# Performance work log

Hardware: AMD Instinct MI355X
Metric: run time of the kernel (lower is better)

The kernel has to match this reference:

```python
import jax, jax.numpy as jnp
import numpy as np

B, N_CAPS, N_VOTES, D_IN, D_H, D_CP = 1024, 64, 36, 256, 128, 32
TWO_PI = 2.0 * np.pi


def geometric_transform(pose):
    # pose: [..., 6] -> affine 3x3 matrix [..., 3, 3] (nonlinear, full affine)
    sx, sy, theta, shear, tx, ty = jnp.split(pose, 6, axis=-1)
    sx = jax.nn.sigmoid(sx) + 1e-2
    sy = jax.nn.sigmoid(sy) + 1e-2
    tx = jnp.tanh(tx * 5.0)
    ty = jnp.tanh(ty * 5.0)
    shear = jnp.tanh(shear * 5.0)
    theta = theta * TWO_PI
    c, s = jnp.cos(theta), jnp.sin(theta)
    row0 = jnp.concatenate([sx * c + shear * sy * s, -sx * s + shear * sy * c, tx], -1)
    row1 = jnp.concatenate([sy * s, sy * c, ty], -1)
    zeros = jnp.zeros_like(tx)
    row2 = jnp.concatenate([zeros, zeros, jnp.ones_like(tx)], -1)
    return jnp.stack([row0, row1, row2], axis=-2)


def setup_inputs() -> dict:
    key = jax.random.key(0)
    ks = jax.random.split(key, 16)
    u = lambda k, shp: 0.5 * (jax.random.uniform(k, shp, jnp.float32) - 0.5)
    return {
        "features": jax.random.normal(ks[0], (B, N_CAPS, D_IN), jnp.float32),
        "w1": u(ks[1], (1, N_CAPS, D_IN, D_H)),
        "b1": jnp.zeros((1, N_CAPS, 1, D_H), jnp.float32),
        "w2": u(ks[2], (1, N_CAPS, D_H, D_CP)),
        "b2": jnp.zeros((1, N_CAPS, 1, D_CP), jnp.float32),
        "caps_mlp_w": u(ks[3], (1, N_CAPS, D_CP + 1, D_H)),
        "caps_mlp_b": jnp.zeros((1, N_CAPS, 1, D_H), jnp.float32),
        "cpr_dynamic_w": u(ks[4], (1, N_CAPS, D_H, N_VOTES * 6)),
        "ccr_w": u(ks[5], (1, N_CAPS, D_H, 6)),
        "ccr_b": jnp.zeros((1, N_CAPS, 1, 6), jnp.float32),
        "pres_caps_w": u(ks[6], (1, N_CAPS, D_H, 1)),
        "pres_caps_b": jnp.zeros((1, N_CAPS, 1, 1), jnp.float32),
        "pres_vote_w": u(ks[7], (1, N_CAPS, D_H, N_VOTES)),
        "pres_vote_b": jnp.zeros((1, N_CAPS, 1, N_VOTES), jnp.float32),
        "scale_vote_w": u(ks[8], (1, N_CAPS, D_H, N_VOTES)),
        "scale_vote_b": jnp.zeros((1, N_CAPS, 1, N_VOTES), jnp.float32),
        "cpr_static": jax.random.uniform(ks[9], (1, N_CAPS, N_VOTES, 6), jnp.float32) - 0.5,
    }


def reference(features, w1, b1, w2, b2, caps_mlp_w, caps_mlp_b, cpr_dynamic_w,
              ccr_w, ccr_b, pres_caps_w, pres_caps_b, pres_vote_w, pres_vote_b,
              scale_vote_w, scale_vote_b, cpr_static):
    batch_size = features.shape[0]
    x = features[:, :, None, :]                               # [B, C, 1, 256]
    h = jax.nn.relu(x @ w1 + b1)                              # [B, C, 1, H]
    raw_caps_params = jax.nn.relu(h @ w2 + b2)                # [B, C, 1, P]
    caps_exist = jnp.ones(raw_caps_params.shape[:-1] + (1,), raw_caps_params.dtype)
    caps_params = jnp.concatenate([raw_caps_params, caps_exist], -1)  # [B, C, 1, P+1]
    caps_feat = jax.nn.relu(caps_params @ caps_mlp_w + caps_mlp_b)    # [B, C, 1, H]

    cpr_dynamic = (caps_feat @ cpr_dynamic_w).reshape(batch_size, N_CAPS, N_VOTES, 6)
    ccr = caps_feat @ ccr_w + ccr_b                           # [B, C, 1, 6]
    pres_logit_per_caps = (caps_feat @ pres_caps_w + pres_caps_b)[:, :, 0, :]   # [B, C, 1]
    pres_logit_per_vote = (caps_feat @ pres_vote_w + pres_vote_b)[:, :, 0, :]   # [B, C, V]
    scale_per_vote = (caps_feat @ scale_vote_w + scale_vote_b)[:, :, 0, :]      # [B, C, V]

    ccr_mat = geometric_transform(ccr)                        # [B, C, 1, 3, 3]
    cpr_mat = geometric_transform(cpr_dynamic + cpr_static)   # [B, C, V, 3, 3]
    votes = ccr_mat @ cpr_mat                                 # [B, C, V, 3, 3]

    pres_per_caps = jax.nn.sigmoid(pres_logit_per_caps)
    pres_per_vote = pres_per_caps * jax.nn.sigmoid(pres_logit_per_vote)
    scale_per_vote = jax.nn.softplus(scale_per_vote + 0.5) + 0.01
    dynamic_weights_l2 = jnp.sum(cpr_dynamic ** 2) / batch_size / 2.0
    return (votes, scale_per_vote, pres_per_vote, pres_logit_per_caps,
            pres_logit_per_vote, dynamic_weights_l2, raw_caps_params[:, :, 0, :], features)
```

## Files before the change

kernel.cpp:

```cpp
#include <hip/hip_runtime.h>
#include <math.h>

#define NB   1024
#define NC   64
#define DIN  256
#define DH   128
#define DCP  32
#define NV   36

#define OFF0 0
#define OFF1 21233664
#define OFF2 23592960
#define OFF3 25952256
#define OFF4 26017792
#define OFF5 28377088
#define OFF6 28377089
#define OFF7 30474241

#define SM_FST 0
#define SM_R2  4608
#define SM_R3  8960
#define SM_TOT 10112

#define SM_XS  SM_R2
#define SM_W1C (SM_R2 + 576)
#define SM_W2S SM_R2
#define SM_WM  SM_R2
#define SM_WH  SM_R2
#define SM_HD  (SM_R2 + 1280)
#define SM_HB  (SM_R2 + 3872)
#define SM_WD  SM_R2
#define SM_DYN SM_R2
#define SM_CPS SM_R3
#define SM_M   SM_R3
#define SM_PSIG (SM_R3 + 192)

__device__ __forceinline__ float sigm(float x) { return 1.0f / (1.0f + __expf(-x)); }
__device__ __forceinline__ float tanh5(float x) {
    x = fminf(fmaxf(5.0f * x, -15.0f), 15.0f);
    float z = __expf(2.0f * x);
    return (z - 1.0f) / (z + 1.0f);
}
__device__ __forceinline__ void geo(const float* p, float* m) {
    float sx = sigm(p[0]) + 0.01f;
    float sy = sigm(p[1]) + 0.01f;
    float th = p[2] * 6.28318530717958647692f;
    float sh = tanh5(p[3]);
    float tx = tanh5(p[4]);
    float ty = tanh5(p[5]);
    float cc = __cosf(th), ss = __sinf(th);
    m[0] =  sx * cc + sh * sy * ss;
    m[1] = -sx * ss + sh * sy * cc;
    m[2] = tx;
    m[3] = sy * ss;
    m[4] = sy * cc;
    m[5] = ty;
}

__global__ void zero_l2_kernel(float* out) { out[OFF5] = 0.0f; }

__global__ __launch_bounds__(256, 4)
void caps_fused_kernel(const float* __restrict__ feat,
                       const float* __restrict__ w1,  const float* __restrict__ b1,
                       const float* __restrict__ w2,  const float* __restrict__ b2,
                       const float* __restrict__ wm,  const float* __restrict__ bm,
                       const float* __restrict__ wdy,
                       const float* __restrict__ wccr,const float* __restrict__ bccr,
                       const float* __restrict__ wpc, const float* __restrict__ bpc,
                       const float* __restrict__ wpv, const float* __restrict__ bpv,
                       const float* __restrict__ wsv, const float* __restrict__ bsv,
                       const float* __restrict__ cst,
                       float* __restrict__ out)
{
    __shared__ float sm[SM_TOT];
    const int t  = threadIdx.x;
    const int c  = blockIdx.y;
    const int rb = blockIdx.x * 32;
    const int t4 = t * 4;

    float4 w2pf[4];

    {
        const int tx = t & 31;
        const int ty = t >> 5;
        const int xrow = t >> 3, xk2 = (t & 7) * 2;
        const float* fsrc = &feat[(rb + xrow) * (NC * DIN) + c * DIN + xk2];
        const float* w1b_ = &w1[c * (DIN * DH)];
        float2 xr  = *(const float2*)fsrc;
        float4 wra = *(const float4*)(w1b_ + t4);
        float4 wrb = *(const float4*)(w1b_ + 1024 + t4);
        float acc[4][4] = {};
        for (int k0 = 0; k0 < DIN; k0 += 16) {
            __syncthreads();
            sm[SM_XS + xk2 * 36 + xrow]       = xr.x;
            sm[SM_XS + (xk2 + 1) * 36 + xrow] = xr.y;
            *(float4*)&sm[SM_W1C + t4]        = wra;
            *(float4*)&sm[SM_W1C + 1024 + t4] = wrb;
            __syncthreads();
            if (k0 + 16 < DIN) {
                xr  = *(const float2*)(fsrc + k0 + 16);
                wra = *(const float4*)(w1b_ + (k0 + 16) * DH + t4);
                wrb = *(const float4*)(w1b_ + (k0 + 16) * DH + 1024 + t4);
            } else {
#pragma unroll
                for (int p = 0; p < 4; ++p)
                    w2pf[p] = *(const float4*)&w2[c * (DH * DCP) + (t + p * 256) * 4];
            }
#pragma unroll
            for (int kk = 0; kk < 16; ++kk) {
                const float4 av = *(const float4*)&sm[SM_XS + kk * 36 + ty * 4];
                const float4 bv = *(const float4*)&sm[SM_W1C + kk * DH + tx * 4];
                acc[0][0] += av.x * bv.x; acc[0][1] += av.x * bv.y; acc[0][2] += av.x * bv.z; acc[0][3] += av.x * bv.w;
                acc[1][0] += av.y * bv.x; acc[1][1] += av.y * bv.y; acc[1][2] += av.y * bv.z; acc[1][3] += av.y * bv.w;
                acc[2][0] += av.z * bv.x; acc[2][1] += av.z * bv.y; acc[2][2] += av.z * bv.z; acc[2][3] += av.z * bv.w;
                acc[3][0] += av.w * bv.x; acc[3][1] += av.w * bv.y; acc[3][2] += av.w * bv.z; acc[3][3] += av.w * bv.w;
            }
        }
        const float4 bb = *(const float4*)&b1[c * DH + tx * 4];
        const float bbA[4] = { bb.x, bb.y, bb.z, bb.w };
#pragma unroll
        for (int j = 0; j < 4; ++j) {
            float4 vv;
            vv.x = fmaxf(acc[0][j] + bbA[j], 0.0f);
            vv.y = fmaxf(acc[1][j] + bbA[j], 0.0f);
            vv.z = fmaxf(acc[2][j] + bbA[j], 0.0f);
            vv.w = fmaxf(acc[3][j] + bbA[j], 0.0f);
            *(float4*)&sm[SM_FST + (tx * 4 + j) * 36 + ty * 4] = vv;
        }
    }

    __syncthreads();
#pragma unroll
    for (int p = 0; p < 4; ++p)
        *(float4*)&sm[SM_W2S + t4 + p * 1024] = w2pf[p];
    __syncthreads();
    float4 wmpf[5];
    {
#pragma unroll
        for (int p = 0; p < 5; ++p) {
            const int idx = t + p * 256;
            if (idx < 1056)
                wmpf[p] = *(const float4*)&wm[c * (33 * DH) + idx * 4];
        }
        const int b  = t & 31;
        const int j4 = (t >> 5) << 2;
        float acc[4] = {};
#pragma unroll 8
        for (int k = 0; k < DH; ++k) {
            const float h = sm[SM_FST + k * 36 + b];
            const float4 wv = *(const float4*)&sm[SM_W2S + k * DCP + j4];
            acc[0] += h * wv.x; acc[1] += h * wv.y; acc[2] += h * wv.z; acc[3] += h * wv.w;
        }
        const float4 b2v = *(const float4*)&b2[c * DCP + j4];
        const float b2A[4] = { b2v.x, b2v.y, b2v.z, b2v.w };
#pragma unroll
        for (int jj = 0; jj < 4; ++jj) {
            const float v = fmaxf(acc[jj] + b2A[jj], 0.0f);
            out[OFF6 + ((rb + b) * NC + c) * DCP + j4 + jj] = v;
            sm[SM_CPS + b * 36 + j4 + jj] = v;
        }
    }

    __syncthreads();
#pragma unroll
    for (int p = 0; p < 5; ++p) {
        const int idx = t + p * 256;
        if (idx < 1056)
            *(float4*)&sm[SM_WM + idx * 4] = wmpf[p];
    }
    __syncthreads();
    const float* d2p[5]; int d2adv[5]; float d2msk[5], d2pf[5];
#pragma unroll
    for (int p = 0; p < 5; ++p) {
        const int idx = t + p * 256;
        const int kp = idx / 80, colp = idx - kp * 80;
        const float* s; int st; float mk = 1.0f;
        if (colp < 6)       { s = &wccr[c * (DH * 6) + kp * 6 + colp];          st = 6;  }
        else if (colp == 6) { s = &wpc [c * DH + kp];                            st = 1;  }
        else if (colp < 43) { s = &wpv [c * (DH * NV) + kp * NV + (colp - 7)];   st = NV; }
        else if (colp < 79) { s = &wsv [c * (DH * NV) + kp * NV + (colp - 43)];  st = NV; }
        else                { s = &wccr[c * (DH * 6)]; st = 0; mk = 0.0f; }
        d2pf[p]  = *s;
        d2p[p]   = s + st * 16;
        d2adv[p] = st * 16;
        d2msk[p] = mk;
    }
    float bpf = 0.0f;
    if (t < 80) {
        if (t < 6)       bpf = bccr[c * 6 + t];
        else if (t == 6) bpf = bpc[c];
        else if (t < 43) bpf = bpv[c * NV + (t - 7)];
        else if (t < 79) bpf = bsv[c * NV + (t - 43)];
    }
    {
        const int b  = t & 31;
        const int nb = (t >> 5) << 4;
        float acc[16] = {};
#pragma unroll
        for (int k4 = 0; k4 < 8; ++k4) {
            const float4 a4 = *(const float4*)&sm[SM_CPS + b * 36 + k4 * 4];
            const float aA[4] = { a4.x, a4.y, a4.z, a4.w };
#pragma unroll
            for (int kk = 0; kk < 4; ++kk) {
                const int k = k4 * 4 + kk;
#pragma unroll
                for (int jq = 0; jq < 4; ++jq) {
                    const float4 wv = *(const float4*)&sm[SM_WM + k * DH + nb + jq * 4];
                    acc[jq*4+0] += aA[kk] * wv.x; acc[jq*4+1] += aA[kk] * wv.y;
                    acc[jq*4+2] += aA[kk] * wv.z; acc[jq*4+3] += aA[kk] * wv.w;
                }
            }
        }
#pragma unroll
        for (int jq = 0; jq < 4; ++jq) {
            const float4 wv = *(const float4*)&sm[SM_WM + 32 * DH + nb + jq * 4];
            acc[jq*4+0] += wv.x; acc[jq*4+1] += wv.y; acc[jq*4+2] += wv.z; acc[jq*4+3] += wv.w;
        }
#pragma unroll
        for (int jq = 0; jq < 4; ++jq) {
            const float4 bmv = *(const float4*)&bm[c * DH + nb + jq * 4];
            sm[SM_FST + (nb + jq*4 + 0) * 36 + b] = fmaxf(acc[jq*4+0] + bmv.x, 0.0f);
            sm[SM_FST + (nb + jq*4 + 1) * 36 + b] = fmaxf(acc[jq*4+1] + bmv.y, 0.0f);
            sm[SM_FST + (nb + jq*4 + 2) * 36 + b] = fmaxf(acc[jq*4+2] + bmv.z, 0.0f);
            sm[SM_FST + (nb + jq*4 + 3) * 36 + b] = fmaxf(acc[jq*4+3] + bmv.w, 0.0f);
        }
    }

    {
        const int txx = t & 15;
        const int tyy = t >> 4;
        float acc[2][5] = {};
        for (int k0 = 0; k0 < DH; k0 += 16) {
            __syncthreads();
#pragma unroll
            for (int p = 0; p < 5; ++p)
                sm[SM_WH + t + p * 256] = d2msk[p] * d2pf[p];
            if (k0 == 0 && t < 80) sm[SM_HB + t] = bpf;
            __syncthreads();
            if (k0 + 16 < DH) {
#pragma unroll
                for (int p = 0; p < 5; ++p) {
                    d2pf[p] = *d2p[p];
                    d2p[p] += d2adv[p];
                }
            }
#pragma unroll
            for (int kk = 0; kk < 16; ++kk) {
                const float2 av = *(const float2*)&sm[SM_FST + (k0 + kk) * 36 + tyy * 2];
#pragma unroll
                for (int j = 0; j < 5; ++j) {
                    const float w = sm[SM_WH + kk * 80 + txx * 5 + j];
                    acc[0][j] += av.x * w;
                    acc[1][j] += av.y * w;
                }
            }
        }
#pragma unroll
        for (int i = 0; i < 2; ++i)
#pragma unroll
            for (int j = 0; j < 5; ++j)
                sm[SM_HD + (tyy * 2 + i) * 81 + txx * 5 + j] = acc[i][j];
    }

    const float* d4p[7]; int d4dst[7]; unsigned d4v = 0; float2 d4pf[7];
    {
        const float* wdyb = &wdy[c * (DH * 216)];
#pragma unroll
        for (int p = 0; p < 7; ++p) {
            const int e2  = (t + p * 256) * 2;
            const int row = e2 / 224, col = e2 - row * 224;
            d4dst[p] = row * 224 + col;
            d4pf[p]  = make_float2(0.0f, 0.0f);
            d4p[p]   = wdyb;
            if (col < 216) {
                d4v |= 1u << p;
                d4p[p]  = wdyb + row * 216 + col;
                d4pf[p] = *(const float2*)d4p[p];
                d4p[p] += 16 * 216;
            }
        }
    }
    __syncthreads();

    if (t < 32) {
        const int b = t;
        const float plc = sm[SM_HD + b * 81 + 6] + sm[SM_HB + 6];
        out[OFF3 + (rb + b) * NC + c] = plc;
        sm[SM_PSIG + b] = sigm(plc);
        float pp[6], m[6];
#pragma unroll
        for (int i = 0; i < 6; ++i) pp[i] = sm[SM_HD + b * 81 + i] + sm[SM_HB + i];
        geo(pp, m);
#pragma unroll
        for (int i = 0; i < 6; ++i) sm[SM_M + b * 6 + i] = m[i];
    }
    __syncthreads();

#pragma unroll
    for (int p = 0; p < 10; ++p) {
        const int item = t + p * 256;
        const int b = item / 80, col = item % 80;
        if (col >= 7 && col < 79) {
            const float v = sm[SM_HD + b * 81 + col] + sm[SM_HB + col];
            const int base = ((rb + b) * NC + c) * NV;
            if (col < 43) {
                const int o = col - 7;
                out[OFF4 + base + o] = v;
                out[OFF2 + base + o] = sm[SM_PSIG + b] * sigm(v);
            } else {
                const int o = col - 43;
                float sp = v + 0.5f;
                sp = (sp > 15.0f) ? sp : log1pf(__expf(sp));
                out[OFF1 + base + o] = sp + 0.01f;
            }
        }
    }

    float l2loc = 0.0f;
    {
        const int g   = t & 63;
        const int ty4 = t >> 6;
        float acc[8][4] = {};
        for (int k0 = 0; k0 < DH; k0 += 16) {
            __syncthreads();
#pragma unroll
            for (int p = 0; p < 7; ++p)
                *(float2*)&sm[SM_WD + d4dst[p]] = d4pf[p];
            __syncthreads();
            if (k0 + 16 < DH) {
#pragma unroll
                for (int p = 0; p < 7; ++p) {
                    if ((d4v >> p) & 1) {
                        d4pf[p] = *(const float2*)d4p[p];
                        d4p[p] += 16 * 216;
                    }
                }
            }
#pragma unroll
            for (int kk = 0; kk < 16; ++kk) {
                const float4 a0 = *(const float4*)&sm[SM_FST + (k0 + kk) * 36 + ty4 * 8];
                const float4 a1 = *(const float4*)&sm[SM_FST + (k0 + kk) * 36 + ty4 * 8 + 4];
                const float4 w  = *(const float4*)&sm[SM_WD + kk * 224 + g * 4];
                acc[0][0] += a0.x * w.x; acc[0][1] += a0.x * w.y; acc[0][2] += a0.x * w.z; acc[0][3] += a0.x * w.w;
                acc[1][0] += a0.y * w.x; acc[1][1] += a0.y * w.y; acc[1][2] += a0.y * w.z; acc[1][3] += a0.y * w.w;
                acc[2][0] += a0.z * w.x; acc[2][1] += a0.z * w.y; acc[2][2] += a0.z * w.z; acc[2][3] += a0.z * w.w;
                acc[3][0] += a0.w * w.x; acc[3][1] += a0.w * w.y; acc[3][2] += a0.w * w.z; acc[3][3] += a0.w * w.w;
                acc[4][0] += a1.x * w.x; acc[4][1] += a1.x * w.y; acc[4][2] += a1.x * w.z; acc[4][3] += a1.x * w.w;
                acc[5][0] += a1.y * w.x; acc[5][1] += a1.y * w.y; acc[5][2] += a1.y * w.z; acc[5][3] += a1.y * w.w;
                acc[6][0] += a1.z * w.x; acc[6][1] += a1.z * w.y; acc[6][2] += a1.z * w.z; acc[6][3] += a1.z * w.w;
                acc[7][0] += a1.w * w.x; acc[7][1] += a1.w * w.y; acc[7][2] += a1.w * w.z; acc[7][3] += a1.w * w.w;
            }
        }
        for (int half = 0; half < 2; ++half) {
            __syncthreads();
            if (g < 54 && (g >= 27) == (half == 1)) {
#pragma unroll
                for (int i = 0; i < 8; ++i)
#pragma unroll
                    for (int j = 0; j < 4; ++j)
                        sm[SM_DYN + (ty4 * 8 + i) * 109 + (g * 4 + j - half * 108)] = acc[i][j];
            }
            __syncthreads();
#pragma unroll
            for (int p = 0; p < 3; ++p) {
                const int item = t + p * 256;
                if (item < 576) {
                    const int b = item / 18, vh = item % 18;
                    const int v = half * 18 + vh;
                    float dyn[6], pose[6], mB[6];
                    float ss = 0.0f;
#pragma unroll
                    for (int j = 0; j < 6; ++j) {
                        dyn[j] = sm[SM_DYN + b * 109 + vh * 6 + j];
                        ss += dyn[j] * dyn[j];
                        pose[j] = dyn[j] + cst[c * (NV * 6) + v * 6 + j];
                    }
                    l2loc += ss;
                    geo(pose, mB);
                    const float A0 = sm[SM_M + b * 6 + 0], A1 = sm[SM_M + b * 6 + 1];
                    const float A2 = sm[SM_M + b * 6 + 2], A3 = sm[SM_M + b * 6 + 3];
                    const float A4 = sm[SM_M + b * 6 + 4], A5 = sm[SM_M + b * 6 + 5];
                    const int ob = (((rb + b) * NC + c) * NV + v) * 9;
                    out[OFF0 + ob + 0] = A0 * mB[0] + A1 * mB[3];
                    out[OFF0 + ob + 1] = A0 * mB[1] + A1 * mB[4];
                    out[OFF0 + ob + 2] = A0 * mB[2] + A1 * mB[5] + A2;
                    out[OFF0 + ob + 3] = A3 * mB[0] + A4 * mB[3];
                    out[OFF0 + ob + 4] = A3 * mB[1] + A4 * mB[4];
                    out[OFF0 + ob + 5] = A3 * mB[2] + A4 * mB[5] + A5;
                    out[OFF0 + ob + 6] = 0.0f;
                    out[OFF0 + ob + 7] = 0.0f;
                    out[OFF0 + ob + 8] = 1.0f;
                }
            }
        }
    }

    l2loc += __shfl_down(l2loc, 32, 64);
    l2loc += __shfl_down(l2loc, 16, 64);
    l2loc += __shfl_down(l2loc, 8, 64);
    l2loc += __shfl_down(l2loc, 4, 64);
    l2loc += __shfl_down(l2loc, 2, 64);
    l2loc += __shfl_down(l2loc, 1, 64);
    if ((t & 63) == 0) atomicAdd(&out[OFF5], l2loc * (1.0f / 2048.0f));
}

extern "C" void kernel_launch(void* const* d_in, const int* in_sizes, int n_in,
                              void* d_out, int out_size, void* d_ws, size_t ws_size,
                              hipStream_t stream)
{
    const float* feat = (const float*)d_in[0];
    const float* w1   = (const float*)d_in[1];
    const float* b1   = (const float*)d_in[2];
    const float* w2   = (const float*)d_in[3];
    const float* b2   = (const float*)d_in[4];
    const float* wm   = (const float*)d_in[5];
    const float* bm   = (const float*)d_in[6];
    const float* wdy  = (const float*)d_in[7];
    const float* wccr = (const float*)d_in[8];
    const float* bccr = (const float*)d_in[9];
    const float* wpc  = (const float*)d_in[10];
    const float* bpc  = (const float*)d_in[11];
    const float* wpv  = (const float*)d_in[12];
    const float* bpv  = (const float*)d_in[13];
    const float* wsv  = (const float*)d_in[14];
    const float* bsv  = (const float*)d_in[15];
    const float* cst  = (const float*)d_in[16];
    float* out = (float*)d_out;

    zero_l2_kernel<<<1, 1, 0, stream>>>(out);
    hipMemcpyAsync((void*)(out + OFF7), (const void*)feat,
                   (size_t)NB * NC * DIN * sizeof(float),
                   hipMemcpyDeviceToDevice, stream);
    dim3 grid(NB / 32, NC);
    caps_fused_kernel<<<grid, 256, 0, stream>>>(feat, w1, b1, w2, b2, wm, bm, wdy,
                                                wccr, bccr, wpc, bpc, wpv, bpv,
                                                wsv, bsv, cst, out);
}
```

Baseline: 653.8 us.

## Split first GEMM over K halves, transpose head weights, fuse feature copy kernel

The first layer GEMM now splits the K dimension across two 128-thread halves. Each thread computes an 8x4 tile, and the two halves' partial sums are combined through an XOR-swizzled shared-memory reduction. The head-weight staging is transposed so the inner loop reads float4 weights and does four K steps per load. The caps_params output is now written with a coalesced pass from shared memory, and the memset plus device-to-device memcpy are replaced by one grid-stride copy kernel. The aim is fewer LDS reads per FMA, better coalescing and less launch overhead, at the cost of extra syncs and a reduction step.

```diff
diff --git a/kernel.cpp b/kernel.cpp
--- a/kernel.cpp
+++ b/kernel.cpp
@@ -24,11 +24,12 @@
 
 #define SM_XS  SM_R2
 #define SM_W1C (SM_R2 + 576)
+#define SM_RED SM_R2
 #define SM_W2S SM_R2
 #define SM_WM  SM_R2
-#define SM_WH  SM_R2
-#define SM_HD  (SM_R2 + 1280)
-#define SM_HB  (SM_R2 + 3872)
+#define SM_WHT SM_R2
+#define SM_HD  (SM_R2 + 1600)
+#define SM_HB  (SM_R2 + 4192)
 #define SM_WD  SM_R2
 #define SM_DYN SM_R2
 #define SM_CPS SM_R3
@@ -57,7 +58,15 @@
     m[5] = ty;
 }
 
-__global__ void zero_l2_kernel(float* out) { out[OFF5] = 0.0f; }
+__global__ __launch_bounds__(256)
+void prep_kernel(const float* __restrict__ feat, float* __restrict__ out)
+{
+    if (blockIdx.x == 0 && threadIdx.x == 0) out[OFF5] = 0.0f;
+    const int n = NB * NC * DIN;
+    const int stride = gridDim.x * 256;
+    for (int i = blockIdx.x * 256 + threadIdx.x; i < n; i += stride)
+        out[OFF7 + i] = feat[i];
+}
 
 __global__ __launch_bounds__(256, 4)
 void caps_fused_kernel(const float* __restrict__ feat,
@@ -76,63 +85,94 @@
     const int t  = threadIdx.x;
     const int c  = blockIdx.y;
     const int rb = blockIdx.x * 32;
-    const int t4 = t * 4;
 
     float4 w2pf[4];
 
     {
-        const int tx = t & 31;
-        const int ty = t >> 5;
-        const int xrow = t >> 3, xk2 = (t & 7) * 2;
-        const float* fsrc = &feat[(rb + xrow) * (NC * DIN) + c * DIN + xk2];
-        const float* w1b_ = &w1[c * (DIN * DH)];
-        float2 xr  = *(const float2*)fsrc;
-        float4 wra = *(const float4*)(w1b_ + t4);
-        float4 wrb = *(const float4*)(w1b_ + 1024 + t4);
-        float acc[4][4] = {};
-        for (int k0 = 0; k0 < DIN; k0 += 16) {
-            __syncthreads();
-            sm[SM_XS + xk2 * 36 + xrow]       = xr.x;
-            sm[SM_XS + (xk2 + 1) * 36 + xrow] = xr.y;
-            *(float4*)&sm[SM_W1C + t4]        = wra;
-            *(float4*)&sm[SM_W1C + 1024 + t4] = wrb;
-            __syncthreads();
-            if (k0 + 16 < DIN) {
-                xr  = *(const float2*)(fsrc + k0 + 16);
-                wra = *(const float4*)(w1b_ + (k0 + 16) * DH + t4);
-                wrb = *(const float4*)(w1b_ + (k0 + 16) * DH + 1024 + t4);
+        const int kh  = t >> 7;
+        const int tid = t & 127;
+        const int rg  = tid >> 5;
+        const int cg  = tid & 31;
+        const int xrow = tid >> 2;
+        const int xk2  = (tid & 3) * 2;
+        const int wrow = tid >> 4;
+        const int wcol = (tid & 15) * 8;
+        const float* fsrc = &feat[(rb + xrow) * (NC * DIN) + c * DIN + kh * 128 + xk2];
+        const float* wsrc = &w1[c * (DIN * DH) + (kh * 128 + wrow) * DH + wcol];
+        float2 xr = *(const float2*)fsrc;
+        float4 wa = *(const float4*)wsrc;
+        float4 wb = *(const float4*)(wsrc + 4);
+        float acc[8][4] = {};
+        const int xbase = SM_XS  + kh * 288;
+        const int wbase = SM_W1C + kh * 1056;
+        for (int k0 = 0; k0 < 128; k0 += 8) {
+            __syncthreads();
+            sm[xbase + xk2 * 36 + xrow]       = xr.x;
+            sm[xbase + (xk2 + 1) * 36 + xrow] = xr.y;
+            *(float4*)&sm[wbase + wrow * 132 + wcol]     = wa;
+            *(float4*)&sm[wbase + wrow * 132 + wcol + 4] = wb;
+            __syncthreads();
+            if (k0 + 8 < 128) {
+                xr = *(const float2*)(fsrc + k0 + 8);
+                wa = *(const float4*)(wsrc + (k0 + 8) * DH);
+                wb = *(const float4*)(wsrc + (k0 + 8) * DH + 4);
             } else {
 #pragma unroll
                 for (int p = 0; p < 4; ++p)
                     w2pf[p] = *(const float4*)&w2[c * (DH * DCP) + (t + p * 256) * 4];
             }
 #pragma unroll
-            for (int kk = 0; kk < 16; ++kk) {
-                const float4 av = *(const float4*)&sm[SM_XS + kk * 36 + ty * 4];
-                const float4 bv = *(const float4*)&sm[SM_W1C + kk * DH + tx * 4];
-                acc[0][0] += av.x * bv.x; acc[0][1] += av.x * bv.y; acc[0][2] += av.x * bv.z; acc[0][3] += av.x * bv.w;
-                acc[1][0] += av.y * bv.x; acc[1][1] += av.y * bv.y; acc[1][2] += av.y * bv.z; acc[1][3] += av.y * bv.w;
-                acc[2][0] += av.z * bv.x; acc[2][1] += av.z * bv.y; acc[2][2] += av.z * bv.z; acc[2][3] += av.z * bv.w;
-                acc[3][0] += av.w * bv.x; acc[3][1] += av.w * bv.y; acc[3][2] += av.w * bv.z; acc[3][3] += av.w * bv.w;
-            }
-        }
-        const float4 bb = *(const float4*)&b1[c * DH + tx * 4];
-        const float bbA[4] = { bb.x, bb.y, bb.z, bb.w };
-#pragma unroll
-        for (int j = 0; j < 4; ++j) {
-            float4 vv;
-            vv.x = fmaxf(acc[0][j] + bbA[j], 0.0f);
-            vv.y = fmaxf(acc[1][j] + bbA[j], 0.0f);
-            vv.z = fmaxf(acc[2][j] + bbA[j], 0.0f);
-            vv.w = fmaxf(acc[3][j] + bbA[j], 0.0f);
-            *(float4*)&sm[SM_FST + (tx * 4 + j) * 36 + ty * 4] = vv;
-        }
-    }
-
-    __syncthreads();
-#pragma unroll
-    for (int p = 0; p < 4; ++p)
-        *(float4*)&sm[SM_W2S + t4 + p * 1024] = w2pf[p];
+            for (int kk = 0; kk < 8; ++kk) {
+                const float4 a0 = *(const float4*)&sm[xbase + kk * 36 + rg * 8];
+                const float4 a1 = *(const float4*)&sm[xbase + kk * 36 + rg * 8 + 4];
+                const float4 bv = *(const float4*)&sm[wbase + kk * 132 + cg * 4];
+                acc[0][0] += a0.x * bv.x; acc[0][1] += a0.x * bv.y; acc[0][2] += a0.x * bv.z; acc[0][3] += a0.x * bv.w;
+                acc[1][0] += a0.y * bv.x; acc[1][1] += a0.y * bv.y; acc[1][2] += a0.y * bv.z; acc[1][3] += a0.y * bv.w;
+                acc[2][0] += a0.z * bv.x; acc[2][1] += a0.z * bv.y; acc[2][2] += a0.z * bv.z; acc[2][3] += a0.z * bv.w;
+                acc[3][0] += a0.w * bv.x; acc[3][1] += a0.w * bv.y; acc[3][2] += a0.w * bv.z; acc[3][3] += a0.w * bv.w;
+                acc[4][0] += a1.x * bv.x; acc[4][1] += a1.x * bv.y; acc[4][2] += a1.x * bv.z; acc[4][3] += a1.x * bv.w;
+                acc[5][0] += a1.y * bv.x; acc[5][1] += a1.y * bv.y; acc[5][2] += a1.y * bv.z; acc[5][3] += a1.y * bv.w;
+                acc[6][0] += a1.z * bv.x; acc[6][1] += a1.z * bv.y; acc[6][2] += a1.z * bv.z; acc[6][3] += a1.z * bv.w;
+                acc[7][0] += a1.w * bv.x; acc[7][1] += a1.w * bv.y; acc[7][2] += a1.w * bv.z; acc[7][3] += a1.w * bv.w;
+            }
+        }
+        __syncthreads();
+        if (kh == 1) {
+#pragma unroll
+            for (int r = 0; r < 8; ++r) {
+                float4 v = make_float4(acc[r][0], acc[r][1], acc[r][2], acc[r][3]);
+                *(float4*)&sm[SM_RED + tid * 32 + ((r ^ (tid & 7)) << 2)] = v;
+            }
+        }
+        __syncthreads();
+        if (kh == 0) {
+            const float4 bb = *(const float4*)&b1[c * DH + cg * 4];
+            const float bbA[4] = { bb.x, bb.y, bb.z, bb.w };
+#pragma unroll
+            for (int r = 0; r < 8; ++r) {
+                const float4 v = *(const float4*)&sm[SM_RED + tid * 32 + ((r ^ (tid & 7)) << 2)];
+                acc[r][0] = fmaxf(acc[r][0] + v.x + bbA[0], 0.0f);
+                acc[r][1] = fmaxf(acc[r][1] + v.y + bbA[1], 0.0f);
+                acc[r][2] = fmaxf(acc[r][2] + v.z + bbA[2], 0.0f);
+                acc[r][3] = fmaxf(acc[r][3] + v.w + bbA[3], 0.0f);
+            }
+#pragma unroll
+            for (int j = 0; j < 4; ++j) {
+                float4 lo = make_float4(acc[0][j], acc[1][j], acc[2][j], acc[3][j]);
+                float4 hi = make_float4(acc[4][j], acc[5][j], acc[6][j], acc[7][j]);
+                *(float4*)&sm[SM_FST + (cg * 4 + j) * 36 + rg * 8]     = lo;
+                *(float4*)&sm[SM_FST + (cg * 4 + j) * 36 + rg * 8 + 4] = hi;
+            }
+        }
+    }
+
+    __syncthreads();
+    {
+        const int t4 = t * 4;
+#pragma unroll
+        for (int p = 0; p < 4; ++p)
+            *(float4*)&sm[SM_W2S + t4 + p * 1024] = w2pf[p];
+    }
     __syncthreads();
     float4 wmpf[5];
     {
@@ -154,11 +194,8 @@
         const float4 b2v = *(const float4*)&b2[c * DCP + j4];
         const float b2A[4] = { b2v.x, b2v.y, b2v.z, b2v.w };
 #pragma unroll
-        for (int jj = 0; jj < 4; ++jj) {
-            const float v = fmaxf(acc[jj] + b2A[jj], 0.0f);
-            out[OFF6 + ((rb + b) * NC + c) * DCP + j4 + jj] = v;
-            sm[SM_CPS + b * 36 + j4 + jj] = v;
-        }
+        for (int jj = 0; jj < 4; ++jj)
+            sm[SM_CPS + b * 36 + j4 + jj] = fmaxf(acc[jj] + b2A[jj], 0.0f);
     }
 
     __syncthreads();
@@ -168,12 +205,19 @@
         if (idx < 1056)
             *(float4*)&sm[SM_WM + idx * 4] = wmpf[p];
     }
-    __syncthreads();
-    const float* d2p[5]; int d2adv[5]; float d2msk[5], d2pf[5];
+#pragma unroll
+    for (int p = 0; p < 4; ++p) {
+        const int item = t + p * 256;
+        const int b = item >> 5, j = item & 31;
+        out[OFF6 + ((rb + b) * NC + c) * DCP + j] = sm[SM_CPS + b * 36 + j];
+    }
+    __syncthreads();
+    const float* d2p[5]; int d2adv[5], d2dst[5]; float d2msk[5], d2pf[5];
 #pragma unroll
     for (int p = 0; p < 5; ++p) {
         const int idx = t + p * 256;
         const int kp = idx / 80, colp = idx - kp * 80;
+        d2dst[p] = colp * 20 + kp;
         const float* s; int st; float mk = 1.0f;
         if (colp < 6)       { s = &wccr[c * (DH * 6) + kp * 6 + colp];          st = 6;  }
         else if (colp == 6) { s = &wpc [c * DH + kp];                            st = 1;  }
@@ -234,7 +278,7 @@
             __syncthreads();
 #pragma unroll
             for (int p = 0; p < 5; ++p)
-                sm[SM_WH + t + p * 256] = d2msk[p] * d2pf[p];
+                sm[SM_WHT + d2dst[p]] = d2msk[p] * d2pf[p];
             if (k0 == 0 && t < 80) sm[SM_HB + t] = bpf;
             __syncthreads();
             if (k0 + 16 < DH) {
@@ -245,13 +289,16 @@
                 }
             }
 #pragma unroll
-            for (int kk = 0; kk < 16; ++kk) {
-                const float2 av = *(const float2*)&sm[SM_FST + (k0 + kk) * 36 + tyy * 2];
+            for (int kb = 0; kb < 16; kb += 4) {
+                float2 av[4];
+#pragma unroll
+                for (int q = 0; q < 4; ++q)
+                    av[q] = *(const float2*)&sm[SM_FST + (k0 + kb + q) * 36 + tyy * 2];
 #pragma unroll
                 for (int j = 0; j < 5; ++j) {
-                    const float w = sm[SM_WH + kk * 80 + txx * 5 + j];
-                    acc[0][j] += av.x * w;
-                    acc[1][j] += av.y * w;
+                    const float4 wv = *(const float4*)&sm[SM_WHT + (txx * 5 + j) * 20 + kb];
+                    acc[0][j] += av[0].x * wv.x + av[1].x * wv.y + av[2].x * wv.z + av[3].x * wv.w;
+                    acc[1][j] += av[0].y * wv.x + av[1].y * wv.y + av[2].y * wv.z + av[3].y * wv.w;
                 }
             }
         }
@@ -427,10 +474,7 @@
     const float* cst  = (const float*)d_in[16];
     float* out = (float*)d_out;
 
-    zero_l2_kernel<<<1, 1, 0, stream>>>(out);
-    hipMemcpyAsync((void*)(out + OFF7), (const void*)feat,
-                   (size_t)NB * NC * DIN * sizeof(float),
-                   hipMemcpyDeviceToDevice, stream);
+    prep_kernel<<<2048, 256, 0, stream>>>(feat, out);
     dim3 grid(NB / 32, NC);
     caps_fused_kernel<<<grid, 256, 0, stream>>>(feat, w1, b1, w2, b2, wm, bm, wdy,
                                                 wccr, bccr, wpc, bpc, wpv, bpv,
```

Measured after the change: 755.6 us. 1.16x slower.

## Double rows per block to 64 and replace memcpy with a copy kernel

Applied to the files above, without the earlier changes.

Each block now handles 64 batch rows with 512 threads instead of 32 rows with 256 threads. Every per-capsule weight tile loaded into shared memory is therefore reused across twice as many rows, which roughly halves global weight traffic and per-block staging overhead. The zero kernel and device-to-device memcpy are merged into one grid-stride copy kernel. The caps_params output is now written through shared memory in a coalesced pattern. The trade-off is a larger shared-memory footprint, which may lower the number of resident blocks per CU, plus more masking logic in the load loops.

```diff
diff --git a/kernel.cpp b/kernel.cpp
--- a/kernel.cpp
+++ b/kernel.cpp
@@ -17,23 +17,27 @@
 #define OFF6 28377089
 #define OFF7 30474241
 
+#define RT   64
+#define THR  512
+
+#define FSS  68
 #define SM_FST 0
-#define SM_R2  4608
-#define SM_R3  8960
-#define SM_TOT 10112
+#define SM_R2  8704
+#define SM_R3  15680
+#define SM_TOT 17984
 
 #define SM_XS  SM_R2
-#define SM_W1C (SM_R2 + 576)
+#define SM_W1C (SM_R2 + 1088)
 #define SM_W2S SM_R2
 #define SM_WM  SM_R2
 #define SM_WH  SM_R2
 #define SM_HD  (SM_R2 + 1280)
-#define SM_HB  (SM_R2 + 3872)
+#define SM_HB  (SM_R2 + 6464)
 #define SM_WD  SM_R2
 #define SM_DYN SM_R2
 #define SM_CPS SM_R3
 #define SM_M   SM_R3
-#define SM_PSIG (SM_R3 + 192)
+#define SM_PSIG (SM_R3 + 384)
 
 __device__ __forceinline__ float sigm(float x) { return 1.0f / (1.0f + __expf(-x)); }
 __device__ __forceinline__ float tanh5(float x) {
@@ -57,9 +61,17 @@
     m[5] = ty;
 }
 
-__global__ void zero_l2_kernel(float* out) { out[OFF5] = 0.0f; }
-
-__global__ __launch_bounds__(256, 4)
+__global__ __launch_bounds__(256)
+void prep_kernel(const float* __restrict__ feat, float* __restrict__ out)
+{
+    if (blockIdx.x == 0 && threadIdx.x == 0) out[OFF5] = 0.0f;
+    const int n = NB * NC * DIN;
+    const int stride = gridDim.x * 256;
+    for (int i = blockIdx.x * 256 + threadIdx.x; i < n; i += stride)
+        out[OFF7 + i] = feat[i];
+}
+
+__global__ __launch_bounds__(THR, 4)
 void caps_fused_kernel(const float* __restrict__ feat,
                        const float* __restrict__ w1,  const float* __restrict__ b1,
                        const float* __restrict__ w2,  const float* __restrict__ b2,
@@ -75,41 +87,37 @@
     __shared__ float sm[SM_TOT];
     const int t  = threadIdx.x;
     const int c  = blockIdx.y;
-    const int rb = blockIdx.x * 32;
-    const int t4 = t * 4;
-
-    float4 w2pf[4];
+    const int rb = blockIdx.x * RT;
+
+    float4 w2pf[2];
 
     {
         const int tx = t & 31;
         const int ty = t >> 5;
-        const int xrow = t >> 3, xk2 = (t & 7) * 2;
+        const int xrow = t >> 3;
+        const int xk2  = (t & 7) * 2;
         const float* fsrc = &feat[(rb + xrow) * (NC * DIN) + c * DIN + xk2];
-        const float* w1b_ = &w1[c * (DIN * DH)];
-        float2 xr  = *(const float2*)fsrc;
-        float4 wra = *(const float4*)(w1b_ + t4);
-        float4 wrb = *(const float4*)(w1b_ + 1024 + t4);
+        const float* wsrc = &w1[c * (DIN * DH) + (t >> 5) * DH + (t & 31) * 4];
+        float2 xr = *(const float2*)fsrc;
+        float4 wr = *(const float4*)wsrc;
         float acc[4][4] = {};
         for (int k0 = 0; k0 < DIN; k0 += 16) {
             __syncthreads();
-            sm[SM_XS + xk2 * 36 + xrow]       = xr.x;
-            sm[SM_XS + (xk2 + 1) * 36 + xrow] = xr.y;
-            *(float4*)&sm[SM_W1C + t4]        = wra;
-            *(float4*)&sm[SM_W1C + 1024 + t4] = wrb;
+            sm[SM_XS + xk2 * FSS + xrow]       = xr.x;
+            sm[SM_XS + (xk2 + 1) * FSS + xrow] = xr.y;
+            *(float4*)&sm[SM_W1C + (t >> 5) * 128 + (t & 31) * 4] = wr;
             __syncthreads();
             if (k0 + 16 < DIN) {
-                xr  = *(const float2*)(fsrc + k0 + 16);
-                wra = *(const float4*)(w1b_ + (k0 + 16) * DH + t4);
-                wrb = *(const float4*)(w1b_ + (k0 + 16) * DH + 1024 + t4);
+                xr = *(const float2*)(fsrc + k0 + 16);
+                wr = *(const float4*)(wsrc + (k0 + 16) * DH);
             } else {
-#pragma unroll
-                for (int p = 0; p < 4; ++p)
-                    w2pf[p] = *(const float4*)&w2[c * (DH * DCP) + (t + p * 256) * 4];
+                w2pf[0] = *(const float4*)&w2[c * (DH * DCP) + t * 4];
+                w2pf[1] = *(const float4*)&w2[c * (DH * DCP) + (t + THR) * 4];
             }
 #pragma unroll
             for (int kk = 0; kk < 16; ++kk) {
-                const float4 av = *(const float4*)&sm[SM_XS + kk * 36 + ty * 4];
-                const float4 bv = *(const float4*)&sm[SM_W1C + kk * DH + tx * 4];
+                const float4 av = *(const float4*)&sm[SM_XS + kk * FSS + ty * 4];
+                const float4 bv = *(const float4*)&sm[SM_W1C + kk * 128 + tx * 4];
                 acc[0][0] += av.x * bv.x; acc[0][1] += av.x * bv.y; acc[0][2] += av.x * bv.z; acc[0][3] += av.x * bv.w;
                 acc[1][0] += av.y * bv.x; acc[1][1] += av.y * bv.y; acc[1][2] += av.y * bv.z; acc[1][3] += av.y * bv.w;
                 acc[2][0] += av.z * bv.x; acc[2][1] += av.z * bv.y; acc[2][2] += av.z * bv.z; acc[2][3] += av.z * bv.w;
@@ -125,65 +133,72 @@
             vv.y = fmaxf(acc[1][j] + bbA[j], 0.0f);
             vv.z = fmaxf(acc[2][j] + bbA[j], 0.0f);
             vv.w = fmaxf(acc[3][j] + bbA[j], 0.0f);
-            *(float4*)&sm[SM_FST + (tx * 4 + j) * 36 + ty * 4] = vv;
-        }
-    }
-
-    __syncthreads();
-#pragma unroll
-    for (int p = 0; p < 4; ++p)
-        *(float4*)&sm[SM_W2S + t4 + p * 1024] = w2pf[p];
-    __syncthreads();
-    float4 wmpf[5];
-    {
-#pragma unroll
-        for (int p = 0; p < 5; ++p) {
-            const int idx = t + p * 256;
+            *(float4*)&sm[SM_FST + (tx * 4 + j) * FSS + ty * 4] = vv;
+        }
+    }
+
+    __syncthreads();
+    *(float4*)&sm[SM_W2S + t * 4]         = w2pf[0];
+    *(float4*)&sm[SM_W2S + (t + THR) * 4] = w2pf[1];
+    __syncthreads();
+    float4 wmpf[3];
+    {
+#pragma unroll
+        for (int p = 0; p < 3; ++p) {
+            const int idx = t + p * THR;
             if (idx < 1056)
                 wmpf[p] = *(const float4*)&wm[c * (33 * DH) + idx * 4];
         }
-        const int b  = t & 31;
-        const int j4 = (t >> 5) << 2;
+        const int b  = t & 63;
+        const int j4 = (t >> 6) << 2;
         float acc[4] = {};
 #pragma unroll 8
         for (int k = 0; k < DH; ++k) {
-            const float h = sm[SM_FST + k * 36 + b];
+            const float h = sm[SM_FST + k * FSS + b];
             const float4 wv = *(const float4*)&sm[SM_W2S + k * DCP + j4];
             acc[0] += h * wv.x; acc[1] += h * wv.y; acc[2] += h * wv.z; acc[3] += h * wv.w;
         }
         const float4 b2v = *(const float4*)&b2[c * DCP + j4];
-        const float b2A[4] = { b2v.x, b2v.y, b2v.z, b2v.w };
-#pragma unroll
-        for (int jj = 0; jj < 4; ++jj) {
-            const float v = fmaxf(acc[jj] + b2A[jj], 0.0f);
-            out[OFF6 + ((rb + b) * NC + c) * DCP + j4 + jj] = v;
-            sm[SM_CPS + b * 36 + j4 + jj] = v;
-        }
-    }
-
-    __syncthreads();
-#pragma unroll
-    for (int p = 0; p < 5; ++p) {
-        const int idx = t + p * 256;
+        float4 cv;
+        cv.x = fmaxf(acc[0] + b2v.x, 0.0f);
+        cv.y = fmaxf(acc[1] + b2v.y, 0.0f);
+        cv.z = fmaxf(acc[2] + b2v.z, 0.0f);
+        cv.w = fmaxf(acc[3] + b2v.w, 0.0f);
+        *(float4*)&sm[SM_CPS + b * 36 + j4] = cv;
+    }
+
+    __syncthreads();
+#pragma unroll
+    for (int p = 0; p < 3; ++p) {
+        const int idx = t + p * THR;
         if (idx < 1056)
             *(float4*)&sm[SM_WM + idx * 4] = wmpf[p];
     }
-    __syncthreads();
-    const float* d2p[5]; int d2adv[5]; float d2msk[5], d2pf[5];
-#pragma unroll
-    for (int p = 0; p < 5; ++p) {
-        const int idx = t + p * 256;
-        const int kp = idx / 80, colp = idx - kp * 80;
-        const float* s; int st; float mk = 1.0f;
-        if (colp < 6)       { s = &wccr[c * (DH * 6) + kp * 6 + colp];          st = 6;  }
-        else if (colp == 6) { s = &wpc [c * DH + kp];                            st = 1;  }
-        else if (colp < 43) { s = &wpv [c * (DH * NV) + kp * NV + (colp - 7)];   st = NV; }
-        else if (colp < 79) { s = &wsv [c * (DH * NV) + kp * NV + (colp - 43)];  st = NV; }
-        else                { s = &wccr[c * (DH * 6)]; st = 0; mk = 0.0f; }
-        d2pf[p]  = *s;
-        d2p[p]   = s + st * 16;
-        d2adv[p] = st * 16;
-        d2msk[p] = mk;
+#pragma unroll
+    for (int p = 0; p < 4; ++p) {
+        const int item = t + p * THR;
+        const int b = item >> 5, j = item & 31;
+        out[OFF6 + ((rb + b) * NC + c) * DCP + j] = sm[SM_CPS + b * 36 + j];
+    }
+    __syncthreads();
+    const float* d2p[3]; int d2adv[3]; float d2msk[3], d2pf[3];
+#pragma unroll
+    for (int p = 0; p < 3; ++p) {
+        const int idx = t + p * THR;
+        d2pf[p] = 0.0f; d2p[p] = wccr; d2adv[p] = 0; d2msk[p] = 0.0f;
+        if (idx < 1280) {
+            const int kp = idx / 80, colp = idx - kp * 80;
+            const float* s; int st; float mk = 1.0f;
+            if (colp < 6)       { s = &wccr[c * (DH * 6) + kp * 6 + colp];          st = 6;  }
+            else if (colp == 6) { s = &wpc [c * DH + kp];                            st = 1;  }
+            else if (colp < 43) { s = &wpv [c * (DH * NV) + kp * NV + (colp - 7)];   st = NV; }
+            else if (colp < 79) { s = &wsv [c * (DH * NV) + kp * NV + (colp - 43)];  st = NV; }
+            else                { s = &wccr[c * (DH * 6)]; st = 0; mk = 0.0f; }
+            d2pf[p]  = *s;
+            d2p[p]   = s + st * 16;
+            d2adv[p] = st * 16;
+            d2msk[p] = mk;
+        }
     }
     float bpf = 0.0f;
     if (t < 80) {
@@ -193,8 +208,8 @@
         else if (t < 79) bpf = bsv[c * NV + (t - 43)];
     }
     {
-        const int b  = t & 31;
-        const int nb = (t >> 5) << 4;
+        const int b  = t & 63;
+        const int nb = (t >> 6) << 4;
         float acc[16] = {};
 #pragma unroll
         for (int k4 = 0; k4 < 8; ++k4) {
@@ -219,10 +234,10 @@
 #pragma unroll
         for (int jq = 0; jq < 4; ++jq) {
             const float4 bmv = *(const float4*)&bm[c * DH + nb + jq * 4];
-            sm[SM_FST + (nb + jq*4 + 0) * 36 + b] = fmaxf(acc[jq*4+0] + bmv.x, 0.0f);
-            sm[SM_FST + (nb + jq*4 + 1) * 36 + b] = fmaxf(acc[jq*4+1] + bmv.y, 0.0f);
-            sm[SM_FST + (nb + jq*4 + 2) * 36 + b] = fmaxf(acc[jq*4+2] + bmv.z, 0.0f);
-            sm[SM_FST + (nb + jq*4 + 3) * 36 + b] = fmaxf(acc[jq*4+3] + bmv.w, 0.0f);
+            sm[SM_FST + (nb + jq*4 + 0) * FSS + b] = fmaxf(acc[jq*4+0] + bmv.x, 0.0f);
+            sm[SM_FST + (nb + jq*4 + 1) * FSS + b] = fmaxf(acc[jq*4+1] + bmv.y, 0.0f);
+            sm[SM_FST + (nb + jq*4 + 2) * FSS + b] = fmaxf(acc[jq*4+2] + bmv.z, 0.0f);
+            sm[SM_FST + (nb + jq*4 + 3) * FSS + b] = fmaxf(acc[jq*4+3] + bmv.w, 0.0f);
         }
     }
 
@@ -233,20 +248,24 @@
         for (int k0 = 0; k0 < DH; k0 += 16) {
             __syncthreads();
 #pragma unroll
-            for (int p = 0; p < 5; ++p)
-                sm[SM_WH + t + p * 256] = d2msk[p] * d2pf[p];
+            for (int p = 0; p < 3; ++p) {
+                const int idx = t + p * THR;
+                if (idx < 1280) sm[SM_WH + idx] = d2msk[p] * d2pf[p];
+            }
             if (k0 == 0 && t < 80) sm[SM_HB + t] = bpf;
             __syncthreads();
             if (k0 + 16 < DH) {
 #pragma unroll
-                for (int p = 0; p < 5; ++p) {
-                    d2pf[p] = *d2p[p];
-                    d2p[p] += d2adv[p];
+                for (int p = 0; p < 3; ++p) {
+                    if (t + p * THR < 1280) {
+                        d2pf[p] = *d2p[p];
+                        d2p[p] += d2adv[p];
+                    }
                 }
             }
 #pragma unroll
             for (int kk = 0; kk < 16; ++kk) {
-                const float2 av = *(const float2*)&sm[SM_FST + (k0 + kk) * 36 + tyy * 2];
+                const float2 av = *(const float2*)&sm[SM_FST + (k0 + kk) * FSS + tyy * 2];
 #pragma unroll
                 for (int j = 0; j < 5; ++j) {
                     const float w = sm[SM_WH + kk * 80 + txx * 5 + j];
@@ -262,27 +281,31 @@
                 sm[SM_HD + (tyy * 2 + i) * 81 + txx * 5 + j] = acc[i][j];
     }
 
-    const float* d4p[7]; int d4dst[7]; unsigned d4v = 0; float2 d4pf[7];
+    const float* d4p[4]; int d4dst[4]; unsigned d4v = 0; float2 d4pf[4];
     {
         const float* wdyb = &wdy[c * (DH * 216)];
 #pragma unroll
-        for (int p = 0; p < 7; ++p) {
-            const int e2  = (t + p * 256) * 2;
-            const int row = e2 / 224, col = e2 - row * 224;
-            d4dst[p] = row * 224 + col;
+        for (int p = 0; p < 4; ++p) {
+            const int i2 = t + p * THR;
+            d4dst[p] = -1;
             d4pf[p]  = make_float2(0.0f, 0.0f);
             d4p[p]   = wdyb;
-            if (col < 216) {
-                d4v |= 1u << p;
-                d4p[p]  = wdyb + row * 216 + col;
-                d4pf[p] = *(const float2*)d4p[p];
-                d4p[p] += 16 * 216;
-            }
-        }
-    }
-    __syncthreads();
-
-    if (t < 32) {
+            if (i2 < 1792) {
+                const int e2  = i2 * 2;
+                const int row = e2 / 224, col = e2 - row * 224;
+                d4dst[p] = row * 224 + col;
+                if (col < 216) {
+                    d4v |= 1u << p;
+                    d4p[p]  = wdyb + row * 216 + col;
+                    d4pf[p] = *(const float2*)d4p[p];
+                    d4p[p] += 16 * 216;
+                }
+            }
+        }
+    }
+    __syncthreads();
+
+    if (t < 64) {
         const int b = t;
         const float plc = sm[SM_HD + b * 81 + 6] + sm[SM_HB + 6];
         out[OFF3 + (rb + b) * NC + c] = plc;
@@ -298,7 +321,7 @@
 
 #pragma unroll
     for (int p = 0; p < 10; ++p) {
-        const int item = t + p * 256;
+        const int item = t + p * THR;
         const int b = item / 80, col = item % 80;
         if (col >= 7 && col < 79) {
             const float v = sm[SM_HD + b * 81 + col] + sm[SM_HB + col];
@@ -319,17 +342,17 @@
     float l2loc = 0.0f;
     {
         const int g   = t & 63;
-        const int ty4 = t >> 6;
+        const int ty8 = t >> 6;
         float acc[8][4] = {};
         for (int k0 = 0; k0 < DH; k0 += 16) {
             __syncthreads();
 #pragma unroll
-            for (int p = 0; p < 7; ++p)
-                *(float2*)&sm[SM_WD + d4dst[p]] = d4pf[p];
+            for (int p = 0; p < 4; ++p)
+                if (d4dst[p] >= 0) *(float2*)&sm[SM_WD + d4dst[p]] = d4pf[p];
             __syncthreads();
             if (k0 + 16 < DH) {
 #pragma unroll
-                for (int p = 0; p < 7; ++p) {
+                for (int p = 0; p < 4; ++p) {
                     if ((d4v >> p) & 1) {
                         d4pf[p] = *(const float2*)d4p[p];
                         d4p[p] += 16 * 216;
@@ -338,8 +361,8 @@
             }
 #pragma unroll
             for (int kk = 0; kk < 16; ++kk) {
-                const float4 a0 = *(const float4*)&sm[SM_FST + (k0 + kk) * 36 + ty4 * 8];
-                const float4 a1 = *(const float4*)&sm[SM_FST + (k0 + kk) * 36 + ty4 * 8 + 4];
+                const float4 a0 = *(const float4*)&sm[SM_FST + (k0 + kk) * FSS + ty8 * 8];
+                const float4 a1 = *(const float4*)&sm[SM_FST + (k0 + kk) * FSS + ty8 * 8 + 4];
                 const float4 w  = *(const float4*)&sm[SM_WD + kk * 224 + g * 4];
                 acc[0][0] += a0.x * w.x; acc[0][1] += a0.x * w.y; acc[0][2] += a0.x * w.z; acc[0][3] += a0.x * w.w;
                 acc[1][0] += a0.y * w.x; acc[1][1] += a0.y * w.y; acc[1][2] += a0.y * w.z; acc[1][3] += a0.y * w.w;
@@ -358,13 +381,13 @@
                 for (int i = 0; i < 8; ++i)
 #pragma unroll
                     for (int j = 0; j < 4; ++j)
-                        sm[SM_DYN + (ty4 * 8 + i) * 109 + (g * 4 + j - half * 108)] = acc[i][j];
+                        sm[SM_DYN + (ty8 * 8 + i) * 109 + (g * 4 + j - half * 108)] = acc[i][j];
             }
             __syncthreads();
 #pragma unroll
             for (int p = 0; p < 3; ++p) {
-                const int item = t + p * 256;
-                if (item < 576) {
+                const int item = t + p * THR;
+                if (item < 1152) {
                     const int b = item / 18, vh = item % 18;
                     const int v = half * 18 + vh;
                     float dyn[6], pose[6], mB[6];
@@ -427,12 +450,9 @@
     const float* cst  = (const float*)d_in[16];
     float* out = (float*)d_out;
 
-    zero_l2_kernel<<<1, 1, 0, stream>>>(out);
-    hipMemcpyAsync((void*)(out + OFF7), (const void*)feat,
-                   (size_t)NB * NC * DIN * sizeof(float),
-                   hipMemcpyDeviceToDevice, stream);
-    dim3 grid(NB / 32, NC);
-    caps_fused_kernel<<<grid, 256, 0, stream>>>(feat, w1, b1, w2, b2, wm, bm, wdy,
+    prep_kernel<<<2048, 256, 0, stream>>>(feat, out);
+    dim3 grid(NB / RT, NC);
+    caps_fused_kernel<<<grid, THR, 0, stream>>>(feat, w1, b1, w2, b2, wm, bm, wdy,
                                                 wccr, bccr, wpc, bpc, wpv, bpv,
                                                 wsv, bsv, cst, out);
 }
```

Result: slower. 1.197 ms (+83.0%).
